# Kernel tuning notes

Measured on AMD Instinct MI355X. Metric: run time of the kernel, lower is better.

Reference implementation:

```python
import jax, jax.numpy as jnp
import numpy as np
from jax import lax

B, L = 8192, 64
N_VALUES, EMBED, HIDDEN, OUT = 1000, 64, 128, 128


def setup_inputs() -> dict:
    key = jax.random.key(0)
    ks = jax.random.split(key, 8)
    s = 0.1  # weight scale ~ 1/sqrt(hidden)
    return {
        "x": jax.random.randint(ks[0], (B, L), 0, N_VALUES),
        "embed": jax.random.normal(ks[1], (N_VALUES, EMBED), jnp.float32) * s,
        "W_ih": jax.random.normal(ks[2], (3 * HIDDEN, EMBED), jnp.float32) * s,
        "W_hh": jax.random.normal(ks[3], (3 * HIDDEN, HIDDEN), jnp.float32) * s,
        "b_ih": jax.random.normal(ks[4], (3 * HIDDEN,), jnp.float32) * s,
        "b_hh": jax.random.normal(ks[5], (3 * HIDDEN,), jnp.float32) * s,
        "W_out": jax.random.normal(ks[6], (OUT, HIDDEN), jnp.float32) * s,
        "b_out": jax.random.normal(ks[7], (OUT,), jnp.float32) * s,
    }


def _gru_encode(x, embed, W_ih, W_hh, b_ih, b_hh, W_out, b_out):
    e = embed[x]  # [B, L, E] embedding lookup
    H = W_hh.shape[1]
    # Precompute input-to-gate projections for all timesteps (batched GEMM).
    xg = jnp.einsum('ble,ge->blg', e, W_ih) + b_ih  # [B, L, 3H]

    def step(h, xg_t):
        hg = h @ W_hh.T + b_hh  # [B, 3H]
        xr, xz, xn = jnp.split(xg_t, 3, axis=-1)
        hr, hz, hn = jnp.split(hg, 3, axis=-1)
        r = jax.nn.sigmoid(xr + hr)
        z = jax.nn.sigmoid(xz + hz)
        n = jnp.tanh(xn + r * hn)  # PyTorch GRU: r gates the hidden 'new' term
        h_new = (1.0 - z) * n + z * h
        return h_new, None

    h0 = jnp.zeros((x.shape[0], H), e.dtype)
    h_last, _ = lax.scan(step, h0, jnp.swapaxes(xg, 0, 1))  # scan over time
    return h_last @ W_out.T + b_out  # [B, OUT]


def reference(x, embed, W_ih, W_hh, b_ih, b_hh, W_out, b_out):
    return _gru_encode(x, embed, W_ih, W_hh, b_ih, b_hh, W_out, b_out)
```

## Files before the change

kernel.cpp:

```cpp
#include <hip/hip_runtime.h>


typedef __bf16 bf16x8 __attribute__((ext_vector_type(8)));
typedef float  f32x4  __attribute__((ext_vector_type(4)));
typedef int    int4v  __attribute__((ext_vector_type(4)));
typedef unsigned int uint4v __attribute__((ext_vector_type(4)));

#define NV   1000
#define EMB  64
#define HD   128
#define G3   384
#define SEQ  64
#define BB   16

#define SC_RZ (-1.4426950408889634f)
#define SC_N  ( 2.8853900817779268f)

__device__ __forceinline__ float bfslot(uint4v w, int s) {
    const unsigned int word = w[s >> 1];
    const unsigned int bits = (s & 1) ? (word & 0xffff0000u) : (word << 16);
    return __builtin_bit_cast(float, bits);
}

__global__ void g_table_kernel(const float* __restrict__ embed,
                               const float* __restrict__ W_ih,
                               const float* __restrict__ b_ih,
                               const float* __restrict__ b_hh,
                               unsigned short* __restrict__ Gpk)
{
    __shared__ float emb[EMB];
    const int v = blockIdx.x;
    const int g = threadIdx.x;
    if (g < EMB) emb[g] = embed[v * EMB + g];
    __syncthreads();
    const float* wr = W_ih + g * EMB;
    float s = b_ih[g] + (g < 2 * HD ? b_hh[g] : 0.f);
    #pragma unroll
    for (int e = 0; e < EMB; e += 4) {
        const float4 w4 = *(const float4*)(wr + e);
        s += w4.x * emb[e] + w4.y * emb[e + 1] + w4.z * emb[e + 2] + w4.w * emb[e + 3];
    }
    const int hid = g & 127, gate = g >> 7;
    s *= (gate < 2) ? SC_RZ : SC_N;
    const int cwi = hid >> 5, hti = (hid >> 4) & 1, c16i = hid & 15;
    Gpk[((v * 4 + cwi) * 16 + c16i) * 8 + (gate + 3 * hti)] =
        __builtin_bit_cast(unsigned short, (__bf16)s);
}

#define GRU_STEP(P, PFU, PFN, T)                                                   \
  {                                                                                \
    int4v tokn = {0, 0, 0, 0};                                                     \
    if ((T) < SEQ - 1) tokn = *(const int4v*)&xl[((T) + 1) * BB + quad * 4];       \
    f32x4 acc[3][2];                                                               \
    float xn_[2][4];                                                               \
    _Pragma("unroll") for (int ht = 0; ht < 2; ++ht)                               \
      _Pragma("unroll") for (int j = 0; j < 4; ++j) {                              \
        acc[0][ht][j] = bfslot(PFU[j], 3 * ht + 0);              \
        acc[1][ht][j] = bfslot(PFU[j], 3 * ht + 1);              \
        acc[2][ht][j] = ht ? bn1 : bn0;                          \
        xn_[ht][j]    = bfslot(PFU[j], 3 * ht + 2);              \
      }                                                                            \
    _Pragma("unroll") for (int ks = 0; ks < 4; ++ks) {                             \
      const bf16x8 af = *(const bf16x8*)(hbase + (P) * 4096 + aoff[ks]);           \
      _Pragma("unroll") for (int gate = 0; gate < 3; ++gate)                       \
        _Pragma("unroll") for (int ht = 0; ht < 2; ++ht)                           \
          acc[gate][ht] = __builtin_amdgcn_mfma_f32_16x16x32_bf16(                 \
              af, wf[gate][ht][ks], acc[gate][ht], 0, 0, 0);                       \
    }                                                                              \
    if ((T) < SEQ - 1) {                                                           \
      _Pragma("unroll") for (int j = 0; j < 4; ++j)                                \
        PFN[j] = *(const uint4v*)(gbase + (unsigned)(tokn[j] * 1024 + goff));      \
    }                                                                              \
    _Pragma("unroll") for (int ht = 0; ht < 2; ++ht) {                             \
      _Pragma("unroll") for (int j = 0; j < 4; ++j) {                              \
        const float r  = __builtin_amdgcn_rcpf(                                    \
            1.f + __builtin_amdgcn_exp2f(acc[0][ht][j]));                          \
        const float zg = __builtin_amdgcn_rcpf(                                    \
            1.f + __builtin_amdgcn_exp2f(acc[1][ht][j]));                          \
        const float v  = __builtin_fmaf(r, acc[2][ht][j], xn_[ht][j]);             \
        const float n  = __builtin_fmaf(-2.f,                                      \
            __builtin_amdgcn_rcpf(1.f + __builtin_amdgcn_exp2f(v)), 1.f);          \
        const float hn = __builtin_fmaf(zg, hreg[ht][j] - n, n);                   \
        hreg[ht][j] = hn;                                                          \
        *(unsigned short*)(hbase + (1 - (P)) * 4096 + woff[ht][j]) =               \
            __builtin_bit_cast(unsigned short, (__bf16)hn);                        \
      }                                                                            \
    }                                                                              \
    asm volatile("s_waitcnt lgkmcnt(0)" ::: "memory");                             \
    __builtin_amdgcn_s_barrier();                                                  \
    __builtin_amdgcn_sched_barrier(0);                                             \
  }

__global__ __launch_bounds__(256, 2) void gru_kernel(
    const int*   __restrict__ x,    const unsigned short* __restrict__ Gpk,
    const float* __restrict__ Whh,  const float* __restrict__ bhh,
    const float* __restrict__ Wout, const float* __restrict__ bout,
    float* __restrict__ out)
{
    __shared__ unsigned short hA[2 * BB * HD];
    __shared__ int xl[SEQ * BB];

    const int tid  = threadIdx.x;
    const int lane = tid & 63;
    const int cw   = tid >> 6;
    const int c16  = lane & 15;
    const int quad = lane >> 4;
    const int br0  = blockIdx.x * BB;

    #pragma unroll
    for (int i = 0; i < 4; ++i) {
        const int r = (tid >> 6) + i * 4;
        const int t = tid & 63;
        xl[t * BB + r] = x[(br0 + r) * SEQ + t];
    }
    #pragma unroll
    for (int i = 0; i < 4; ++i)
        ((unsigned int*)hA)[tid + i * 256] = 0u;

    bf16x8 wf[3][2][4];
    #pragma unroll
    for (int gate = 0; gate < 3; ++gate)
    #pragma unroll
    for (int ht = 0; ht < 2; ++ht)
    #pragma unroll
    for (int ks = 0; ks < 4; ++ks) {
        const float sc = (gate < 2) ? SC_RZ : SC_N;
        const int col = gate * HD + cw * 32 + ht * 16 + c16;
        const float* p = Whh + col * HD + ks * 32 + quad * 4;
        const float4 a = *(const float4*)p;
        const float4 b = *(const float4*)(p + 16);
        bf16x8 f;
        f[0] = (__bf16)(sc * a.x); f[1] = (__bf16)(sc * a.y);
        f[2] = (__bf16)(sc * a.z); f[3] = (__bf16)(sc * a.w);
        f[4] = (__bf16)(sc * b.x); f[5] = (__bf16)(sc * b.y);
        f[6] = (__bf16)(sc * b.z); f[7] = (__bf16)(sc * b.w);
        wf[gate][ht][ks] = f;
    }

    const float bn0 = SC_N * bhh[2 * HD + cw * 32 + c16];
    const float bn1 = SC_N * bhh[2 * HD + cw * 32 + 16 + c16];

    int aoff[4];
    #pragma unroll
    for (int ks = 0; ks < 4; ++ks)
        aoff[ks] = c16 * 256 + ((ks * 64 + quad * 16) ^ ((c16 & 7) << 4));
    int woff[2][4];
    #pragma unroll
    for (int ht = 0; ht < 2; ++ht)
    #pragma unroll
    for (int j = 0; j < 4; ++j) {
        const int hid  = cw * 32 + ht * 16 + c16;
        const int sidx = ((hid >> 5) << 5) | (((hid & 15) >> 2) << 3)
                       | (((hid >> 4) & 1) << 2) | (hid & 3);
        const int row  = quad * 4 + j;
        woff[ht][j] = row * 256 + ((sidx * 2) ^ ((row & 7) << 4));
    }

    char* hbase = (char*)hA;
    const char* gbase = (const char*)Gpk;
    const int goff = cw * 256 + c16 * 16;

    float hreg[2][4] = {{0.f, 0.f, 0.f, 0.f}, {0.f, 0.f, 0.f, 0.f}};
    const f32x4 z4 = {0.f, 0.f, 0.f, 0.f};

    __syncthreads();

    uint4v pfA[4], pfB[4];
    {
        const int4v tok0 = *(const int4v*)&xl[0 * BB + quad * 4];
        #pragma unroll
        for (int j = 0; j < 4; ++j)
            pfA[j] = *(const uint4v*)(gbase + (unsigned)(tok0[j] * 1024 + goff));
    }

    for (int tt = 0; tt < SEQ; tt += 2) {
        GRU_STEP(0, pfA, pfB, tt);
        GRU_STEP(1, pfB, pfA, tt + 1);
    }

    bf16x8 wo[2][4];
    #pragma unroll
    for (int ht = 0; ht < 2; ++ht)
    #pragma unroll
    for (int ks = 0; ks < 4; ++ks) {
        const int col = cw * 32 + ht * 16 + c16;
        const float* p = Wout + col * HD + ks * 32 + quad * 4;
        const float4 a = *(const float4*)p;
        const float4 b = *(const float4*)(p + 16);
        bf16x8 f;
        f[0] = (__bf16)a.x; f[1] = (__bf16)a.y; f[2] = (__bf16)a.z; f[3] = (__bf16)a.w;
        f[4] = (__bf16)b.x; f[5] = (__bf16)b.y; f[6] = (__bf16)b.z; f[7] = (__bf16)b.w;
        wo[ht][ks] = f;
    }
    const float bo0 = bout[cw * 32 + c16];
    const float bo1 = bout[cw * 32 + 16 + c16];

    f32x4 oacc[2] = {z4, z4};
    #pragma unroll
    for (int ks = 0; ks < 4; ++ks) {
        const bf16x8 af = *(const bf16x8*)(hbase + aoff[ks]);
        #pragma unroll
        for (int ht = 0; ht < 2; ++ht)
            oacc[ht] = __builtin_amdgcn_mfma_f32_16x16x32_bf16(af, wo[ht][ks], oacc[ht], 0, 0, 0);
    }
    #pragma unroll
    for (int ht = 0; ht < 2; ++ht) {
        const float bo_ = ht ? bo1 : bo0;
        #pragma unroll
        for (int j = 0; j < 4; ++j) {
            const int row = br0 + quad * 4 + j;
            out[row * HD + cw * 32 + ht * 16 + c16] = oacc[ht][j] + bo_;
        }
    }
}

extern "C" void kernel_launch(void* const* d_in, const int* in_sizes, int n_in,
                              void* d_out, int out_size, void* d_ws, size_t ws_size,
                              hipStream_t stream) {
    const int*   x     = (const int*)  d_in[0];
    const float* embed = (const float*)d_in[1];
    const float* W_ih  = (const float*)d_in[2];
    const float* W_hh  = (const float*)d_in[3];
    const float* b_ih  = (const float*)d_in[4];
    const float* b_hh  = (const float*)d_in[5];
    const float* W_out = (const float*)d_in[6];
    const float* b_out = (const float*)d_in[7];
    float* outp = (float*)d_out;
    unsigned short* Gpk = (unsigned short*)d_ws;

    const int Bsz = in_sizes[0] / SEQ;

    g_table_kernel<<<NV, G3, 0, stream>>>(embed, W_ih, b_ih, b_hh, Gpk);
    gru_kernel<<<Bsz / BB, 256, 0, stream>>>(x, Gpk, W_hh, b_hh, W_out, b_out, outp);
}
```

Before: 103.1 us.

## Process two 16-row batch tiles per block to reuse W_hh fragments

Each block now handles 32 batch rows as two independent 16-row sub-tiles, each with its own h buffers, prefetch registers and hidden-state registers. Both sub-tiles share the register-resident W_hh fragments. Per-step MFMA work doubles per block while the per-step barrier cost is amortised over twice the rows, and the second chain gives the scheduler independent work to interleave. In exchange the grid is halved (256 blocks) and launch bounds drop to one block per SIMD set, which cuts occupancy and may leave CUs idle.

```diff
diff --git a/kernel.cpp b/kernel.cpp
--- a/kernel.cpp
+++ b/kernel.cpp
@@ -11,7 +11,7 @@
 #define HD   128
 #define G3   384
 #define SEQ  64
-#define BB   16
+#define BB   32
 
 #define SC_RZ (-1.4426950408889634f)
 #define SC_N  ( 2.8853900817779268f)
@@ -47,57 +47,76 @@
         __builtin_bit_cast(unsigned short, (__bf16)s);
 }
 
-#define GRU_STEP(P, PFU, PFN, T)                                                   \
-  {                                                                                \
-    int4v tokn = {0, 0, 0, 0};                                                     \
-    if ((T) < SEQ - 1) tokn = *(const int4v*)&xl[((T) + 1) * BB + quad * 4];       \
-    f32x4 acc[3][2];                                                               \
-    float xn_[2][4];                                                               \
+#define GRU_PW(A, XN, HR, TOFF, P)                                                 \
     _Pragma("unroll") for (int ht = 0; ht < 2; ++ht)                               \
       _Pragma("unroll") for (int j = 0; j < 4; ++j) {                              \
-        acc[0][ht][j] = bfslot(PFU[j], 3 * ht + 0);              \
-        acc[1][ht][j] = bfslot(PFU[j], 3 * ht + 1);              \
-        acc[2][ht][j] = ht ? bn1 : bn0;                          \
-        xn_[ht][j]    = bfslot(PFU[j], 3 * ht + 2);              \
+        const float r  = __builtin_amdgcn_rcpf(                                    \
+            1.f + __builtin_amdgcn_exp2f(A[0][ht][j]));                            \
+        const float zg = __builtin_amdgcn_rcpf(                                    \
+            1.f + __builtin_amdgcn_exp2f(A[1][ht][j]));                            \
+        const float v  = __builtin_fmaf(r, A[2][ht][j], XN[ht][j]);                \
+        const float n  = __builtin_fmaf(-2.f,                                      \
+            __builtin_amdgcn_rcpf(1.f + __builtin_amdgcn_exp2f(v)), 1.f);          \
+        const float hn = __builtin_fmaf(zg, HR[ht][j] - n, n);                     \
+        HR[ht][j] = hn;                                                            \
+        *(unsigned short*)(hbase + (TOFF) + (1 - (P)) * 4096 + woff[ht][j]) =      \
+            __builtin_bit_cast(unsigned short, (__bf16)hn);                        \
+      }
+
+#define GRU_STEP(P, T)                                                             \
+  {                                                                                \
+    int4v tk0 = {0, 0, 0, 0}, tk1 = {0, 0, 0, 0};                                  \
+    if ((T) < SEQ - 1) {                                                           \
+      tk0 = *(const int4v*)&xl[((T) + 1) * BB + quad * 4];                         \
+      tk1 = *(const int4v*)&xl[((T) + 1) * BB + 16 + quad * 4];                    \
+    }                                                                              \
+    f32x4 a0[3][2], a1[3][2];                                                      \
+    float xn0[2][4], xn1[2][4];                                                    \
+    _Pragma("unroll") for (int ht = 0; ht < 2; ++ht)                               \
+      _Pragma("unroll") for (int j = 0; j < 4; ++j) {                              \
+        a0[0][ht][j] = bfslot(pf0[j], 3 * ht + 0);                                 \
+        a0[1][ht][j] = bfslot(pf0[j], 3 * ht + 1);                                 \
+        a0[2][ht][j] = ht ? bn1 : bn0;                                             \
+        xn0[ht][j]   = bfslot(pf0[j], 3 * ht + 2);                                 \
+        a1[0][ht][j] = bfslot(pf1[j], 3 * ht + 0);                                 \
+        a1[1][ht][j] = bfslot(pf1[j], 3 * ht + 1);                                 \
+        a1[2][ht][j] = ht ? bn1 : bn0;                                             \
+        xn1[ht][j]   = bfslot(pf1[j], 3 * ht + 2);                                 \
       }                                                                            \
     _Pragma("unroll") for (int ks = 0; ks < 4; ++ks) {                             \
       const bf16x8 af = *(const bf16x8*)(hbase + (P) * 4096 + aoff[ks]);           \
       _Pragma("unroll") for (int gate = 0; gate < 3; ++gate)                       \
         _Pragma("unroll") for (int ht = 0; ht < 2; ++ht)                           \
-          acc[gate][ht] = __builtin_amdgcn_mfma_f32_16x16x32_bf16(                 \
-              af, wf[gate][ht][ks], acc[gate][ht], 0, 0, 0);                       \
+          a0[gate][ht] = __builtin_amdgcn_mfma_f32_16x16x32_bf16(                  \
+              af, wf[gate][ht][ks], a0[gate][ht], 0, 0, 0);                        \
+    }                                                                              \
+    _Pragma("unroll") for (int ks = 0; ks < 4; ++ks) {                             \
+      const bf16x8 af = *(const bf16x8*)(hbase + 8192 + (P) * 4096 + aoff[ks]);    \
+      _Pragma("unroll") for (int gate = 0; gate < 3; ++gate)                       \
+        _Pragma("unroll") for (int ht = 0; ht < 2; ++ht)                           \
+          a1[gate][ht] = __builtin_amdgcn_mfma_f32_16x16x32_bf16(                  \
+              af, wf[gate][ht][ks], a1[gate][ht], 0, 0, 0);                        \
     }                                                                              \
     if ((T) < SEQ - 1) {                                                           \
       _Pragma("unroll") for (int j = 0; j < 4; ++j)                                \
-        PFN[j] = *(const uint4v*)(gbase + (unsigned)(tokn[j] * 1024 + goff));      \
-    }                                                                              \
-    _Pragma("unroll") for (int ht = 0; ht < 2; ++ht) {                             \
-      _Pragma("unroll") for (int j = 0; j < 4; ++j) {                              \
-        const float r  = __builtin_amdgcn_rcpf(                                    \
-            1.f + __builtin_amdgcn_exp2f(acc[0][ht][j]));                          \
-        const float zg = __builtin_amdgcn_rcpf(                                    \
-            1.f + __builtin_amdgcn_exp2f(acc[1][ht][j]));                          \
-        const float v  = __builtin_fmaf(r, acc[2][ht][j], xn_[ht][j]);             \
-        const float n  = __builtin_fmaf(-2.f,                                      \
-            __builtin_amdgcn_rcpf(1.f + __builtin_amdgcn_exp2f(v)), 1.f);          \
-        const float hn = __builtin_fmaf(zg, hreg[ht][j] - n, n);                   \
-        hreg[ht][j] = hn;                                                          \
-        *(unsigned short*)(hbase + (1 - (P)) * 4096 + woff[ht][j]) =               \
-            __builtin_bit_cast(unsigned short, (__bf16)hn);                        \
-      }                                                                            \
-    }                                                                              \
+        pf0[j] = *(const uint4v*)(gbase + (unsigned)(tk0[j] * 1024 + goff));       \
+      _Pragma("unroll") for (int j = 0; j < 4; ++j)                                \
+        pf1[j] = *(const uint4v*)(gbase + (unsigned)(tk1[j] * 1024 + goff));       \
+    }                                                                              \
+    GRU_PW(a0, xn0, hreg0, 0, P)                                                   \
+    GRU_PW(a1, xn1, hreg1, 8192, P)                                                \
     asm volatile("s_waitcnt lgkmcnt(0)" ::: "memory");                             \
     __builtin_amdgcn_s_barrier();                                                  \
     __builtin_amdgcn_sched_barrier(0);                                             \
   }
 
-__global__ __launch_bounds__(256, 2) void gru_kernel(
+__global__ __launch_bounds__(256, 1) void gru_kernel(
     const int*   __restrict__ x,    const unsigned short* __restrict__ Gpk,
     const float* __restrict__ Whh,  const float* __restrict__ bhh,
     const float* __restrict__ Wout, const float* __restrict__ bout,
     float* __restrict__ out)
 {
-    __shared__ unsigned short hA[2 * BB * HD];
+    __shared__ unsigned short hA[2 * 2 * 16 * HD];
     __shared__ int xl[SEQ * BB];
 
     const int tid  = threadIdx.x;
@@ -108,14 +127,20 @@
     const int br0  = blockIdx.x * BB;
 
     #pragma unroll
-    for (int i = 0; i < 4; ++i) {
-        const int r = (tid >> 6) + i * 4;
-        const int t = tid & 63;
+    for (int i = 0; i < 8; ++i) {
+        const int idx = i * 256 + tid;
+        const int r = idx >> 6;
+        const int t = idx & 63;
         xl[t * BB + r] = x[(br0 + r) * SEQ + t];
     }
-    #pragma unroll
-    for (int i = 0; i < 4; ++i)
-        ((unsigned int*)hA)[tid + i * 256] = 0u;
+    {
+        unsigned int* hA32 = (unsigned int*)hA;
+        #pragma unroll
+        for (int i = 0; i < 4; ++i) {
+            hA32[tid + i * 256] = 0u;
+            hA32[2048 + tid + i * 256] = 0u;
+        }
+    }
 
     bf16x8 wf[3][2][4];
     #pragma unroll
@@ -160,22 +185,27 @@
     const char* gbase = (const char*)Gpk;
     const int goff = cw * 256 + c16 * 16;
 
-    float hreg[2][4] = {{0.f, 0.f, 0.f, 0.f}, {0.f, 0.f, 0.f, 0.f}};
+    float hreg0[2][4] = {{0.f, 0.f, 0.f, 0.f}, {0.f, 0.f, 0.f, 0.f}};
+    float hreg1[2][4] = {{0.f, 0.f, 0.f, 0.f}, {0.f, 0.f, 0.f, 0.f}};
     const f32x4 z4 = {0.f, 0.f, 0.f, 0.f};
 
     __syncthreads();
 
-    uint4v pfA[4], pfB[4];
+    uint4v pf0[4], pf1[4];
     {
-        const int4v tok0 = *(const int4v*)&xl[0 * BB + quad * 4];
+        const int4v t0 = *(const int4v*)&xl[0 * BB + quad * 4];
+        const int4v t1 = *(const int4v*)&xl[0 * BB + 16 + quad * 4];
         #pragma unroll
         for (int j = 0; j < 4; ++j)
-            pfA[j] = *(const uint4v*)(gbase + (unsigned)(tok0[j] * 1024 + goff));
+            pf0[j] = *(const uint4v*)(gbase + (unsigned)(t0[j] * 1024 + goff));
+        #pragma unroll
+        for (int j = 0; j < 4; ++j)
+            pf1[j] = *(const uint4v*)(gbase + (unsigned)(t1[j] * 1024 + goff));
     }
 
     for (int tt = 0; tt < SEQ; tt += 2) {
-        GRU_STEP(0, pfA, pfB, tt);
-        GRU_STEP(1, pfB, pfA, tt + 1);
+        GRU_STEP(0, tt);
+        GRU_STEP(1, tt + 1);
     }
 
     bf16x8 wo[2][4];
@@ -195,21 +225,26 @@
     const float bo0 = bout[cw * 32 + c16];
     const float bo1 = bout[cw * 32 + 16 + c16];
 
-    f32x4 oacc[2] = {z4, z4};
+    f32x4 oacc0[2] = {z4, z4}, oacc1[2] = {z4, z4};
     #pragma unroll
     for (int ks = 0; ks < 4; ++ks) {
-        const bf16x8 af = *(const bf16x8*)(hbase + aoff[ks]);
-        #pragma unroll
-        for (int ht = 0; ht < 2; ++ht)
-            oacc[ht] = __builtin_amdgcn_mfma_f32_16x16x32_bf16(af, wo[ht][ks], oacc[ht], 0, 0, 0);
+        const bf16x8 af0 = *(const bf16x8*)(hbase + aoff[ks]);
+        const bf16x8 af1 = *(const bf16x8*)(hbase + 8192 + aoff[ks]);
+        #pragma unroll
+        for (int ht = 0; ht < 2; ++ht) {
+            oacc0[ht] = __builtin_amdgcn_mfma_f32_16x16x32_bf16(af0, wo[ht][ks], oacc0[ht], 0, 0, 0);
+            oacc1[ht] = __builtin_amdgcn_mfma_f32_16x16x32_bf16(af1, wo[ht][ks], oacc1[ht], 0, 0, 0);
+        }
     }
     #pragma unroll
     for (int ht = 0; ht < 2; ++ht) {
         const float bo_ = ht ? bo1 : bo0;
+        const int col = cw * 32 + ht * 16 + c16;
         #pragma unroll
         for (int j = 0; j < 4; ++j) {
             const int row = br0 + quad * 4 + j;
-            out[row * HD + cw * 32 + ht * 16 + c16] = oacc[ht][j] + bo_;
+            out[row * HD + col] = oacc0[ht][j] + bo_;
+            out[(row + 16) * HD + col] = oacc1[ht][j] + bo_;
         }
     }
 }
```

After: 128.5 us. 1.25x slower.

## Split GRU hidden columns across eight waves per block instead of four

Applied to the files above, without the earlier changes.

Each block now runs 512 threads (8 waves), and each wave owns 16 hidden columns instead of 32. This halves the per-wave MFMA chain and gate math on each serial timestep, and the gate table is repacked to 4 bf16 per column so the per-step gather shrinks to 8-byte loads. Launch bounds rise to 512x4, which limits registers per thread. The per-step barrier now synchronises twice as many waves.

```diff
diff --git a/kernel.cpp b/kernel.cpp
--- a/kernel.cpp
+++ b/kernel.cpp
@@ -4,7 +4,7 @@
 typedef __bf16 bf16x8 __attribute__((ext_vector_type(8)));
 typedef float  f32x4  __attribute__((ext_vector_type(4)));
 typedef int    int4v  __attribute__((ext_vector_type(4)));
-typedef unsigned int uint4v __attribute__((ext_vector_type(4)));
+typedef unsigned int uint2v __attribute__((ext_vector_type(2)));
 
 #define NV   1000
 #define EMB  64
@@ -16,10 +16,11 @@
 #define SC_RZ (-1.4426950408889634f)
 #define SC_N  ( 2.8853900817779268f)
 
-__device__ __forceinline__ float bfslot(uint4v w, int s) {
-    const unsigned int word = w[s >> 1];
-    const unsigned int bits = (s & 1) ? (word & 0xffff0000u) : (word << 16);
-    return __builtin_bit_cast(float, bits);
+__device__ __forceinline__ float bflo(unsigned int word) {
+    return __builtin_bit_cast(float, word << 16);
+}
+__device__ __forceinline__ float bfhi(unsigned int word) {
+    return __builtin_bit_cast(float, word & 0xffff0000u);
 }
 
 __global__ void g_table_kernel(const float* __restrict__ embed,
@@ -42,56 +43,52 @@
     }
     const int hid = g & 127, gate = g >> 7;
     s *= (gate < 2) ? SC_RZ : SC_N;
-    const int cwi = hid >> 5, hti = (hid >> 4) & 1, c16i = hid & 15;
-    Gpk[((v * 4 + cwi) * 16 + c16i) * 8 + (gate + 3 * hti)] =
+    const int w8 = hid >> 4, c16i = hid & 15;
+    Gpk[((v * 8 + w8) * 16 + c16i) * 4 + gate] =
         __builtin_bit_cast(unsigned short, (__bf16)s);
 }
 
-#define GRU_STEP(P, PFU, PFN, T)                                                   \
+#define GRU_STEP(P, T)                                                             \
   {                                                                                \
-    int4v tokn = {0, 0, 0, 0};                                                     \
-    if ((T) < SEQ - 1) tokn = *(const int4v*)&xl[((T) + 1) * BB + quad * 4];       \
-    f32x4 acc[3][2];                                                               \
-    float xn_[2][4];                                                               \
-    _Pragma("unroll") for (int ht = 0; ht < 2; ++ht)                               \
-      _Pragma("unroll") for (int j = 0; j < 4; ++j) {                              \
-        acc[0][ht][j] = bfslot(PFU[j], 3 * ht + 0);              \
-        acc[1][ht][j] = bfslot(PFU[j], 3 * ht + 1);              \
-        acc[2][ht][j] = ht ? bn1 : bn0;                          \
-        xn_[ht][j]    = bfslot(PFU[j], 3 * ht + 2);              \
-      }                                                                            \
+    int4v tk = {0, 0, 0, 0};                                                       \
+    if ((T) < SEQ - 1) tk = *(const int4v*)&xl[((T) + 1) * BB + quad * 4];         \
+    f32x4 acc[3];                                                                  \
+    float xn_[4];                                                                  \
+    _Pragma("unroll") for (int j = 0; j < 4; ++j) {                                \
+      acc[0][j] = bflo(pf[j][0]);                                         \
+      acc[1][j] = bfhi(pf[j][0]);                                         \
+      acc[2][j] = bnw;                                                    \
+      xn_[j]    = bflo(pf[j][1]);                                         \
+    }                                                                              \
     _Pragma("unroll") for (int ks = 0; ks < 4; ++ks) {                             \
       const bf16x8 af = *(const bf16x8*)(hbase + (P) * 4096 + aoff[ks]);           \
       _Pragma("unroll") for (int gate = 0; gate < 3; ++gate)                       \
-        _Pragma("unroll") for (int ht = 0; ht < 2; ++ht)                           \
-          acc[gate][ht] = __builtin_amdgcn_mfma_f32_16x16x32_bf16(                 \
-              af, wf[gate][ht][ks], acc[gate][ht], 0, 0, 0);                       \
+        acc[gate] = __builtin_amdgcn_mfma_f32_16x16x32_bf16(                       \
+            af, wf[gate][ks], acc[gate], 0, 0, 0);                                 \
     }                                                                              \
     if ((T) < SEQ - 1) {                                                           \
       _Pragma("unroll") for (int j = 0; j < 4; ++j)                                \
-        PFN[j] = *(const uint4v*)(gbase + (unsigned)(tokn[j] * 1024 + goff));      \
-    }                                                                              \
-    _Pragma("unroll") for (int ht = 0; ht < 2; ++ht) {                             \
-      _Pragma("unroll") for (int j = 0; j < 4; ++j) {                              \
-        const float r  = __builtin_amdgcn_rcpf(                                    \
-            1.f + __builtin_amdgcn_exp2f(acc[0][ht][j]));                          \
-        const float zg = __builtin_amdgcn_rcpf(                                    \
-            1.f + __builtin_amdgcn_exp2f(acc[1][ht][j]));                          \
-        const float v  = __builtin_fmaf(r, acc[2][ht][j], xn_[ht][j]);             \
-        const float n  = __builtin_fmaf(-2.f,                                      \
-            __builtin_amdgcn_rcpf(1.f + __builtin_amdgcn_exp2f(v)), 1.f);          \
-        const float hn = __builtin_fmaf(zg, hreg[ht][j] - n, n);                   \
-        hreg[ht][j] = hn;                                                          \
-        *(unsigned short*)(hbase + (1 - (P)) * 4096 + woff[ht][j]) =               \
-            __builtin_bit_cast(unsigned short, (__bf16)hn);                        \
-      }                                                                            \
+        pf[j] = *(const uint2v*)(gbase + (unsigned)(tk[j] * 1024 + goff));         \
+    }                                                                              \
+    _Pragma("unroll") for (int j = 0; j < 4; ++j) {                                \
+      const float r  = __builtin_amdgcn_rcpf(                                      \
+          1.f + __builtin_amdgcn_exp2f(acc[0][j]));                                \
+      const float zg = __builtin_amdgcn_rcpf(                                      \
+          1.f + __builtin_amdgcn_exp2f(acc[1][j]));                                \
+      const float v  = __builtin_fmaf(r, acc[2][j], xn_[j]);                       \
+      const float n  = __builtin_fmaf(-2.f,                                        \
+          __builtin_amdgcn_rcpf(1.f + __builtin_amdgcn_exp2f(v)), 1.f);            \
+      const float hn = __builtin_fmaf(zg, hreg[j] - n, n);                         \
+      hreg[j] = hn;                                                                \
+      *(unsigned short*)(hbase + (1 - (P)) * 4096 + woff[j]) =                     \
+          __builtin_bit_cast(unsigned short, (__bf16)hn);                          \
     }                                                                              \
     asm volatile("s_waitcnt lgkmcnt(0)" ::: "memory");                             \
     __builtin_amdgcn_s_barrier();                                                  \
     __builtin_amdgcn_sched_barrier(0);                                             \
   }
 
-__global__ __launch_bounds__(256, 2) void gru_kernel(
+__global__ __launch_bounds__(512, 4) void gru_kernel(
     const int*   __restrict__ x,    const unsigned short* __restrict__ Gpk,
     const float* __restrict__ Whh,  const float* __restrict__ bhh,
     const float* __restrict__ Wout, const float* __restrict__ bout,
@@ -102,30 +99,32 @@
 
     const int tid  = threadIdx.x;
     const int lane = tid & 63;
-    const int cw   = tid >> 6;
+    const int w    = tid >> 6;
     const int c16  = lane & 15;
     const int quad = lane >> 4;
     const int br0  = blockIdx.x * BB;
 
     #pragma unroll
-    for (int i = 0; i < 4; ++i) {
-        const int r = (tid >> 6) + i * 4;
-        const int t = tid & 63;
+    for (int i = 0; i < 2; ++i) {
+        const int idx = i * 512 + tid;
+        const int r = idx >> 6;
+        const int t = idx & 63;
         xl[t * BB + r] = x[(br0 + r) * SEQ + t];
     }
-    #pragma unroll
-    for (int i = 0; i < 4; ++i)
-        ((unsigned int*)hA)[tid + i * 256] = 0u;
-
-    bf16x8 wf[3][2][4];
+    {
+        unsigned int* hA32 = (unsigned int*)hA;
+        #pragma unroll
+        for (int i = 0; i < 2; ++i)
+            hA32[i * 512 + tid] = 0u;
+    }
+
+    bf16x8 wf[3][4];
     #pragma unroll
     for (int gate = 0; gate < 3; ++gate)
-    #pragma unroll
-    for (int ht = 0; ht < 2; ++ht)
     #pragma unroll
     for (int ks = 0; ks < 4; ++ks) {
         const float sc = (gate < 2) ? SC_RZ : SC_N;
-        const int col = gate * HD + cw * 32 + ht * 16 + c16;
+        const int col = gate * HD + w * 16 + c16;
         const float* p = Whh + col * HD + ks * 32 + quad * 4;
         const float4 a = *(const float4*)p;
         const float4 b = *(const float4*)(p + 16);
@@ -134,83 +133,73 @@
         f[2] = (__bf16)(sc * a.z); f[3] = (__bf16)(sc * a.w);
         f[4] = (__bf16)(sc * b.x); f[5] = (__bf16)(sc * b.y);
         f[6] = (__bf16)(sc * b.z); f[7] = (__bf16)(sc * b.w);
-        wf[gate][ht][ks] = f;
-    }
-
-    const float bn0 = SC_N * bhh[2 * HD + cw * 32 + c16];
-    const float bn1 = SC_N * bhh[2 * HD + cw * 32 + 16 + c16];
+        wf[gate][ks] = f;
+    }
+
+    const float bnw = SC_N * bhh[2 * HD + w * 16 + c16];
 
     int aoff[4];
     #pragma unroll
     for (int ks = 0; ks < 4; ++ks)
         aoff[ks] = c16 * 256 + ((ks * 64 + quad * 16) ^ ((c16 & 7) << 4));
-    int woff[2][4];
-    #pragma unroll
-    for (int ht = 0; ht < 2; ++ht)
-    #pragma unroll
-    for (int j = 0; j < 4; ++j) {
-        const int hid  = cw * 32 + ht * 16 + c16;
+    int woff[4];
+    {
+        const int hid  = w * 16 + c16;
         const int sidx = ((hid >> 5) << 5) | (((hid & 15) >> 2) << 3)
                        | (((hid >> 4) & 1) << 2) | (hid & 3);
-        const int row  = quad * 4 + j;
-        woff[ht][j] = row * 256 + ((sidx * 2) ^ ((row & 7) << 4));
+        #pragma unroll
+        for (int j = 0; j < 4; ++j) {
+            const int row = quad * 4 + j;
+            woff[j] = row * 256 + ((sidx * 2) ^ ((row & 7) << 4));
+        }
     }
 
     char* hbase = (char*)hA;
     const char* gbase = (const char*)Gpk;
-    const int goff = cw * 256 + c16 * 16;
-
-    float hreg[2][4] = {{0.f, 0.f, 0.f, 0.f}, {0.f, 0.f, 0.f, 0.f}};
+    const int goff = w * 128 + c16 * 8;
+
+    float hreg[4] = {0.f, 0.f, 0.f, 0.f};
     const f32x4 z4 = {0.f, 0.f, 0.f, 0.f};
 
     __syncthreads();
 
-    uint4v pfA[4], pfB[4];
+    uint2v pf[4];
     {
-        const int4v tok0 = *(const int4v*)&xl[0 * BB + quad * 4];
+        const int4v tk0 = *(const int4v*)&xl[0 * BB + quad * 4];
         #pragma unroll
         for (int j = 0; j < 4; ++j)
-            pfA[j] = *(const uint4v*)(gbase + (unsigned)(tok0[j] * 1024 + goff));
+            pf[j] = *(const uint2v*)(gbase + (unsigned)(tk0[j] * 1024 + goff));
     }
 
     for (int tt = 0; tt < SEQ; tt += 2) {
-        GRU_STEP(0, pfA, pfB, tt);
-        GRU_STEP(1, pfB, pfA, tt + 1);
-    }
-
-    bf16x8 wo[2][4];
-    #pragma unroll
-    for (int ht = 0; ht < 2; ++ht)
+        GRU_STEP(0, tt);
+        GRU_STEP(1, tt + 1);
+    }
+
+    bf16x8 wo[4];
     #pragma unroll
     for (int ks = 0; ks < 4; ++ks) {
-        const int col = cw * 32 + ht * 16 + c16;
+        const int col = w * 16 + c16;
         const float* p = Wout + col * HD + ks * 32 + quad * 4;
         const float4 a = *(const float4*)p;
         const float4 b = *(const float4*)(p + 16);
         bf16x8 f;
         f[0] = (__bf16)a.x; f[1] = (__bf16)a.y; f[2] = (__bf16)a.z; f[3] = (__bf16)a.w;
         f[4] = (__bf16)b.x; f[5] = (__bf16)b.y; f[6] = (__bf16)b.z; f[7] = (__bf16)b.w;
-        wo[ht][ks] = f;
-    }
-    const float bo0 = bout[cw * 32 + c16];
-    const float bo1 = bout[cw * 32 + 16 + c16];
-
-    f32x4 oacc[2] = {z4, z4};
+        wo[ks] = f;
+    }
+    const float bow = bout[w * 16 + c16];
+
+    f32x4 oacc = z4;
     #pragma unroll
     for (int ks = 0; ks < 4; ++ks) {
         const bf16x8 af = *(const bf16x8*)(hbase + aoff[ks]);
-        #pragma unroll
-        for (int ht = 0; ht < 2; ++ht)
-            oacc[ht] = __builtin_amdgcn_mfma_f32_16x16x32_bf16(af, wo[ht][ks], oacc[ht], 0, 0, 0);
-    }
-    #pragma unroll
-    for (int ht = 0; ht < 2; ++ht) {
-        const float bo_ = ht ? bo1 : bo0;
-        #pragma unroll
-        for (int j = 0; j < 4; ++j) {
-            const int row = br0 + quad * 4 + j;
-            out[row * HD + cw * 32 + ht * 16 + c16] = oacc[ht][j] + bo_;
-        }
+        oacc = __builtin_amdgcn_mfma_f32_16x16x32_bf16(af, wo[ks], oacc, 0, 0, 0);
+    }
+    #pragma unroll
+    for (int j = 0; j < 4; ++j) {
+        const int row = br0 + quad * 4 + j;
+        out[row * HD + w * 16 + c16] = oacc[j] + bow;
     }
 }
 
@@ -231,5 +220,5 @@
     const int Bsz = in_sizes[0] / SEQ;
 
     g_table_kernel<<<NV, G3, 0, stream>>>(embed, W_ih, b_ih, b_hh, Gpk);
-    gru_kernel<<<Bsz / BB, 256, 0, stream>>>(x, Gpk, W_hh, b_hh, W_out, b_out, outp);
-}
+    gru_kernel<<<Bsz / BB, 512, 0, stream>>>(x, Gpk, W_hh, b_hh, W_out, b_out, outp);
+}
```

Result: faster. 98.12 us (-4.8%).
